# Performance work log

Hardware: AMD Instinct MI355X
Metric: run time of the kernel (lower is better)

Reference implementation:

```python
import jax, jax.numpy as jnp
import numpy as np

B, T, DIN, DOUT = 32, 3136, 192, 384
H, QS, WS = 6, 4, 16            # heads, q_stride, window_size (post-pool)
HD = DOUT // H                   # head_dim = 64
INNER = QS * WS                  # tokens per mask unit before pooling = 64
NW = T // INNER                  # num_windows = 49
MLP_HID = 4 * DOUT
EPS = 1e-5


def layer_norm(x, w, b):
    mu = x.mean(-1, keepdims=True)
    var = ((x - mu) ** 2).mean(-1, keepdims=True)
    return (x - mu) * jax.lax.rsqrt(var + EPS) * w + b


def setup_inputs() -> dict:
    key = jax.random.key(0)
    ks = jax.random.split(key, 16)
    rn = lambda k, shp, fan: jax.random.normal(k, shp, jnp.float32) * (fan ** -0.5)
    return {
        "embeddings": jax.random.normal(ks[0], (B, T, DIN), jnp.float32),
        "norm1_w": jnp.ones((DIN,), jnp.float32),
        "norm1_b": jnp.zeros((DIN,), jnp.float32),
        "w_qkv": rn(ks[1], (3 * DOUT, DIN), DIN),
        "b_qkv": jnp.zeros((3 * DOUT,), jnp.float32),
        "w_attn_proj": rn(ks[2], (DOUT, DOUT), DOUT),
        "b_attn_proj": jnp.zeros((DOUT,), jnp.float32),
        "w_res_proj": rn(ks[3], (DOUT, DIN), DIN),
        "b_res_proj": jnp.zeros((DOUT,), jnp.float32),
        "norm2_w": jnp.ones((DOUT,), jnp.float32),
        "norm2_b": jnp.zeros((DOUT,), jnp.float32),
        "w_fc1": rn(ks[4], (MLP_HID, DOUT), DOUT),
        "b_fc1": jnp.zeros((MLP_HID,), jnp.float32),
        "w_fc2": rn(ks[5], (DOUT, MLP_HID), MLP_HID),
        "b_fc2": jnp.zeros((DOUT,), jnp.float32),
    }


def _block(embeddings, norm1_w, norm1_b, w_qkv, b_qkv, w_attn_proj, b_attn_proj,
           w_res_proj, b_res_proj, norm2_w, norm2_b, w_fc1, b_fc1, w_fc2, b_fc2):
    x = layer_norm(embeddings, norm1_w, norm1_b)                 # [B,T,DIN]

    # residual path: project then do_pool (max over q_stride groups)
    res = x @ w_res_proj.T + b_res_proj                          # [B,T,DOUT]
    res = res.reshape(B, QS, T // QS, DOUT).max(axis=1)          # [B,T/QS,DOUT]

    # mask-unit attention
    qkv = x @ w_qkv.T + b_qkv                                    # [B,T,3*DOUT]
    qkv = qkv.reshape(B, INNER, NW, 3, H, HD)
    qkv = jnp.transpose(qkv, (3, 0, 4, 2, 1, 5))                 # [3,B,H,NW,INNER,HD]
    q, k, v = qkv[0], qkv[1], qkv[2]
    q = q.reshape(B, H, NW, QS, WS, HD).max(axis=3)              # q-pool -> [B,H,NW,WS,HD]
    scale = HD ** -0.5
    attn = jax.nn.softmax(jnp.einsum("bhwqd,bhwkd->bhwqk", q * scale, k), axis=-1)
    out = jnp.einsum("bhwqk,bhwkd->bhwqd", attn, v)              # [B,H,NW,WS,HD]
    out = jnp.transpose(out, (0, 3, 2, 1, 4)).reshape(B, WS * NW, DOUT)
    out = out @ w_attn_proj.T + b_attn_proj

    emb = res + out
    h = layer_norm(emb, norm2_w, norm2_b)
    h = jax.nn.gelu(h @ w_fc1.T + b_fc1, approximate=False)
    emb = emb + (h @ w_fc2.T + b_fc2)
    return emb, attn


def reference(embeddings, norm1_w, norm1_b, w_qkv, b_qkv, w_attn_proj, b_attn_proj,
              w_res_proj, b_res_proj, norm2_w, norm2_b, w_fc1, b_fc1, w_fc2, b_fc2):
    return _block(embeddings, norm1_w, norm1_b, w_qkv, b_qkv, w_attn_proj, b_attn_proj,
                  w_res_proj, b_res_proj, norm2_w, norm2_b, w_fc1, b_fc1, w_fc2, b_fc2)
```

## Files before the change

kernel.cpp:

```cpp
#include <hip/hip_runtime.h>
#include <stdint.h>

typedef __bf16 bf16_t;
typedef __attribute__((ext_vector_type(8))) __bf16 bf16x8;
typedef __attribute__((ext_vector_type(4))) __bf16 bf16x4;
typedef __attribute__((ext_vector_type(4))) float f32x4;

#define NB_ 32
#define NT_ 3136
#define DIN_ 192
#define DOUT_ 384
#define NH_ 6
#define HD_ 64
#define NW_ 49
#define WSZ_ 16
#define TP_ 784
#define MLP_ 1536

__device__ __forceinline__ f32x4 mfma16(bf16x8 a, bf16x8 b, f32x4 c) {
  return __builtin_amdgcn_mfma_f32_16x16x32_bf16(a, b, c, 0, 0, 0);
}

__device__ __forceinline__ void gload_lds16(const bf16_t* g, bf16_t* l) {
  __builtin_amdgcn_global_load_lds(
      (const __attribute__((address_space(1))) void*)((const void*)g),
      (__attribute__((address_space(3))) void*)l, 16, 0, 0);
}

__device__ __forceinline__ float gelu_tanh(float v) {
  const float t2 = 1.5957691216f * (v + 0.044715f * v * v * v);
  return v * (1.f - 1.f / (1.f + __expf(t2)));
}

__global__ void cvt_kernel(const float* __restrict__ s0, const float* __restrict__ s1,
                           const float* __restrict__ s2, const float* __restrict__ s3,
                           const float* __restrict__ s4, bf16_t* __restrict__ d0,
                           bf16_t* __restrict__ d1, bf16_t* __restrict__ d2,
                           bf16_t* __restrict__ d3, bf16_t* __restrict__ d4) {
  const int b = blockIdx.x;
  const float* s; bf16_t* d; long off;
  if (b < 108)      { s = s0; d = d0; off = (long)b * 2048; }
  else if (b < 144) { s = s1; d = d1; off = (long)(b - 108) * 2048; }
  else if (b < 216) { s = s2; d = d2; off = (long)(b - 144) * 2048; }
  else if (b < 504) { s = s3; d = d3; off = (long)(b - 216) * 2048; }
  else              { s = s4; d = d4; off = (long)(b - 504) * 2048; }
  off += (long)threadIdx.x * 8;
  const float4 a = *(const float4*)(s + off);
  const float4 c = *(const float4*)(s + off + 4);
  bf16x8 o;
  o[0] = (bf16_t)a.x; o[1] = (bf16_t)a.y; o[2] = (bf16_t)a.z; o[3] = (bf16_t)a.w;
  o[4] = (bf16_t)c.x; o[5] = (bf16_t)c.y; o[6] = (bf16_t)c.z; o[7] = (bf16_t)c.w;
  *(bf16x8*)(d + off) = o;
}

template <int D>
__global__ void ln_f32_kernel(const float* __restrict__ in, const float* __restrict__ w,
                              const float* __restrict__ bvec, bf16_t* __restrict__ out) {
  const int row = blockIdx.x * 4 + (threadIdx.x >> 6);
  const int lane = threadIdx.x & 63;
  constexpr int PER = D / 64;
  const float* x = in + (long)row * D;
  float v[PER];
  float s = 0.f;
#pragma unroll
  for (int i = 0; i < PER; i++) { v[i] = x[lane * PER + i]; s += v[i]; }
#pragma unroll
  for (int off = 1; off < 64; off <<= 1) s += __shfl_xor(s, off);
  const float mu = s * (1.f / D);
  float s2 = 0.f;
#pragma unroll
  for (int i = 0; i < PER; i++) { const float d = v[i] - mu; s2 += d * d; }
#pragma unroll
  for (int off = 1; off < 64; off <<= 1) s2 += __shfl_xor(s2, off);
  const float rstd = rsqrtf(s2 * (1.f / D) + 1e-5f);
  bf16_t* o = out + (long)row * D;
#pragma unroll
  for (int i = 0; i < PER; i++) {
    const int c = lane * PER + i;
    o[c] = (bf16_t)((v[i] - mu) * rstd * w[c] + bvec[c]);
  }
}

template <int D>
__global__ void ln_bf16_kernel(const bf16_t* __restrict__ in, const float* __restrict__ w,
                               const float* __restrict__ bvec, bf16_t* __restrict__ out) {
  const int row = blockIdx.x * 4 + (threadIdx.x >> 6);
  const int lane = threadIdx.x & 63;
  constexpr int PER = D / 64;
  const bf16_t* x = in + (long)row * D;
  float v[PER];
  float s = 0.f;
#pragma unroll
  for (int i = 0; i < PER; i++) { v[i] = (float)x[lane * PER + i]; s += v[i]; }
#pragma unroll
  for (int off = 1; off < 64; off <<= 1) s += __shfl_xor(s, off);
  const float mu = s * (1.f / D);
  float s2 = 0.f;
#pragma unroll
  for (int i = 0; i < PER; i++) { const float d = v[i] - mu; s2 += d * d; }
#pragma unroll
  for (int off = 1; off < 64; off <<= 1) s2 += __shfl_xor(s2, off);
  const float rstd = rsqrtf(s2 * (1.f / D) + 1e-5f);
  bf16_t* o = out + (long)row * D;
#pragma unroll
  for (int i = 0; i < PER; i++) {
    const int c = lane * PER + i;
    o[c] = (bf16_t)((v[i] - mu) * rstd * w[c] + bvec[c]);
  }
}

template <int ACT, int POOL>
__global__ __launch_bounds__(512, 4) void gemm8(
    const bf16_t* __restrict__ A, const bf16_t* __restrict__ W,
    const float* __restrict__ bias, bf16_t* __restrict__ C,
    int M, int N, int K) {
  __shared__ __align__(16) char AsB[256 * 128];
  __shared__ __align__(16) char WsB[128 * 128];

  const int nwg = gridDim.x;
  const int q = nwg >> 3, rm = nwg & 7;
  const int xcd = blockIdx.x & 7, idx = blockIdx.x >> 3;
  const int wg = (xcd < rm ? xcd * (q + 1) : rm * (q + 1) + (xcd - rm) * q) + idx;

  const int nbn = N >> 7;
  const int bmi = wg / nbn;
  const int bni = wg - bmi * nbn;
  const int m0 = bmi << 8, n0 = bni << 7;
  const int tid = threadIdx.x;
  const int lane = tid & 63;
  const int wid = tid >> 6;
  const int wr = (wid >> 1) * 64, wc = (wid & 1) * 64;
  const int l15 = lane & 15;
  const int lkb = (lane >> 4) << 4;
  const int srow = tid >> 3;
  const int scolsw = ((tid & 7) << 3) ^ ((srow & 7) << 3);
  const int swzr = (l15 & 7) << 4;

  f32x4 acc[4][4];
  const f32x4 zero = {0.f, 0.f, 0.f, 0.f};
#pragma unroll
  for (int i = 0; i < 4; i++)
#pragma unroll
    for (int j = 0; j < 4; j++) acc[i][j] = zero;

  long arow[4];
#pragma unroll
  for (int p = 0; p < 4; p++) {
    const int m = m0 + p * 64 + srow;
    if constexpr (POOL) {
      const int b = m / NT_;
      const int mm = m - b * NT_;
      arow[p] = (long)b * NT_ + (mm & 3) * TP_ + (mm >> 2);
    } else {
      arow[p] = m;
    }
  }
  long wrow[2];
#pragma unroll
  for (int p = 0; p < 2; p++) wrow[p] = (long)(n0 + p * 64 + srow);

  for (int k0 = 0; k0 < K; k0 += 64) {
    __syncthreads();
#pragma unroll
    for (int p = 0; p < 4; p++)
      gload_lds16(A + arow[p] * K + k0 + scolsw, (bf16_t*)(AsB + p * 8192 + tid * 16));
#pragma unroll
    for (int p = 0; p < 2; p++)
      gload_lds16(W + wrow[p] * K + k0 + scolsw, (bf16_t*)(WsB + p * 8192 + tid * 16));
    __syncthreads();
#pragma unroll
    for (int kk = 0; kk < 2; kk++) {
      bf16x8 af[4], wf[4];
#pragma unroll
      for (int i = 0; i < 4; i++)
        af[i] = *(const bf16x8*)(AsB + (wr + i * 16 + l15) * 128 + ((kk * 64 + lkb) ^ swzr));
#pragma unroll
      for (int j = 0; j < 4; j++)
        wf[j] = *(const bf16x8*)(WsB + (wc + j * 16 + l15) * 128 + ((kk * 64 + lkb) ^ swzr));
#pragma unroll
      for (int i = 0; i < 4; i++)
#pragma unroll
        for (int j = 0; j < 4; j++) {
          if constexpr (POOL) acc[i][j] = mfma16(af[i], wf[j], acc[i][j]);
          else                acc[i][j] = mfma16(wf[j], af[i], acc[i][j]);
        }
    }
  }

  const int rg = (lane >> 4) * 4;
  if constexpr (POOL) {
#pragma unroll
    for (int j = 0; j < 4; j++) {
      const int gn = n0 + wc + j * 16 + l15;
      const float bv = bias[gn];
#pragma unroll
      for (int i = 0; i < 4; i++) {
        const float v = fmaxf(fmaxf(acc[i][j][0], acc[i][j][1]),
                              fmaxf(acc[i][j][2], acc[i][j][3])) + bv;
        const long pm = (long)((m0 + wr + i * 16 + rg) >> 2);
        C[pm * N + gn] = (bf16_t)v;
      }
    }
  } else {
    __syncthreads();
    char* scr = AsB + wid * 4096;
#pragma unroll
    for (int i = 0; i < 4; i++) {
#pragma unroll
      for (int j = 0; j < 4; j++)
        *(f32x4*)(scr + l15 * 256 + ((((j * 16 + rg) << 2)) ^ ((l15 & 7) << 4))) = acc[i][j];
#pragma unroll
      for (int k = 0; k < 4; k++) {
        const int rl = k * 4 + (lane >> 4);
        const int cb = (lane & 15) << 4;
        const f32x4 v = *(const f32x4*)(scr + rl * 256 + (cb ^ ((rl & 7) << 4)));
        const long gm = m0 + wr + i * 16 + rl;
        const int gn = n0 + wc + ((lane & 15) << 2);
        const float4 bv = *(const float4*)(bias + gn);
        float vv[4] = {v[0] + bv.x, v[1] + bv.y, v[2] + bv.z, v[3] + bv.w};
        if constexpr (ACT == 1) {
#pragma unroll
          for (int r = 0; r < 4; r++) vv[r] = gelu_tanh(vv[r]);
        }
        bf16x4 o;
#pragma unroll
        for (int r = 0; r < 4; r++) o[r] = (bf16_t)vv[r];
        *(bf16x4*)(C + gm * N + gn) = o;
      }
    }
  }
}

template <int HASRES, int OF32, int RF32>
__global__ __launch_bounds__(256) void gemm_t(
    const bf16_t* __restrict__ A, const bf16_t* __restrict__ W,
    const float* __restrict__ bias, const void* __restrict__ resv,
    void* __restrict__ Cv, int M, int N, int K) {
  constexpr int BM = 64;
  constexpr int PA = BM / 32;
  constexpr int ABYTES = BM * 128;
  constexpr int BUFSZ = ABYTES + 128 * 128;
  __shared__ __align__(16) char LDSB[2 * BUFSZ];

  const int nwg = gridDim.x;
  const int q = nwg >> 3, rm = nwg & 7;
  const int xcd = blockIdx.x & 7, idx = blockIdx.x >> 3;
  const int wg = (xcd < rm ? xcd * (q + 1) : rm * (q + 1) + (xcd - rm) * q) + idx;

  const int nbn = N >> 7;
  const int bmi = wg / nbn;
  const int bni = wg - bmi * nbn;
  const int m0 = bmi * BM, n0 = bni << 7;
  const int tid = threadIdx.x;
  const int lane = tid & 63;
  const int wid = tid >> 6;
  const int wr = (wid >> 1) * 32, wc = (wid & 1) * 64;
  const int l15 = lane & 15;
  const int lkb = (lane >> 4) << 4;
  const int srow = tid >> 3;
  const int scolsw = ((tid & 7) << 3) ^ ((srow & 7) << 3);
  const int swzr = (l15 & 7) << 4;

  f32x4 acc[PA][4];
  const f32x4 zero = {0.f, 0.f, 0.f, 0.f};
#pragma unroll
  for (int i = 0; i < PA; i++)
#pragma unroll
    for (int j = 0; j < 4; j++) acc[i][j] = zero;

  long arow[PA];
#pragma unroll
  for (int p = 0; p < PA; p++) arow[p] = m0 + srow + p * 32;
  long wrow[4];
#pragma unroll
  for (int p = 0; p < 4; p++) wrow[p] = (long)(n0 + srow + p * 32);

  auto stage = [&](int buf, int k0) {
    char* base = LDSB + buf * BUFSZ;
#pragma unroll
    for (int p = 0; p < PA; p++)
      gload_lds16(A + arow[p] * K + k0 + scolsw, (bf16_t*)(base + p * 4096 + tid * 16));
#pragma unroll
    for (int p = 0; p < 4; p++)
      gload_lds16(W + wrow[p] * K + k0 + scolsw,
                  (bf16_t*)(base + ABYTES + p * 4096 + tid * 16));
  };

  const int nt = K >> 6;
  stage(0, 0);
  int cur = 0;
  for (int t = 0; t < nt; t++) {
    __syncthreads();
    if (t + 1 < nt) stage(cur ^ 1, (t + 1) << 6);
    const char* base = LDSB + cur * BUFSZ;
#pragma unroll
    for (int kk = 0; kk < 2; kk++) {
      bf16x8 af[PA], wf[4];
#pragma unroll
      for (int i = 0; i < PA; i++)
        af[i] = *(const bf16x8*)(base + (wr + i * 16 + l15) * 128 + ((kk * 64 + lkb) ^ swzr));
#pragma unroll
      for (int j = 0; j < 4; j++)
        wf[j] = *(const bf16x8*)(base + ABYTES + (wc + j * 16 + l15) * 128 +
                                 ((kk * 64 + lkb) ^ swzr));
#pragma unroll
      for (int i = 0; i < PA; i++)
#pragma unroll
        for (int j = 0; j < 4; j++) acc[i][j] = mfma16(wf[j], af[i], acc[i][j]);
    }
    cur ^= 1;
  }

  __syncthreads();
  char* scr = LDSB + wid * 8192;
  const int rg = (lane >> 4) * 4;
#pragma unroll
  for (int i = 0; i < PA; i++) {
    const int ml = i * 16 + l15;
#pragma unroll
    for (int j = 0; j < 4; j++)
      *(f32x4*)(scr + ml * 256 + ((((j * 16 + rg) << 2)) ^ ((ml & 7) << 4))) = acc[i][j];
  }
#pragma unroll
  for (int k = 0; k < 8; k++) {
    const int rl = k * 4 + (lane >> 4);
    const int cb = (lane & 15) << 4;
    const f32x4 v = *(const f32x4*)(scr + rl * 256 + (cb ^ ((rl & 7) << 4)));
    const long gm = m0 + wr + rl;
    const int gn = n0 + wc + ((lane & 15) << 2);
    const float4 bv = *(const float4*)(bias + gn);
    float vv[4] = {v[0] + bv.x, v[1] + bv.y, v[2] + bv.z, v[3] + bv.w};
    if constexpr (HASRES) {
      if constexpr (RF32) {
        const float4 rv = *(const float4*)((const float*)resv + gm * N + gn);
        vv[0] += rv.x; vv[1] += rv.y; vv[2] += rv.z; vv[3] += rv.w;
      } else {
        const bf16x4 rv = *(const bf16x4*)((const bf16_t*)resv + gm * N + gn);
#pragma unroll
        for (int r = 0; r < 4; r++) vv[r] += (float)rv[r];
      }
    }
    if constexpr (OF32) {
      float4 o = {vv[0], vv[1], vv[2], vv[3]};
      *(float4*)((float*)Cv + gm * N + gn) = o;
    } else {
      bf16x4 o;
#pragma unroll
      for (int r = 0; r < 4; r++) o[r] = (bf16_t)vv[r];
      *(bf16x4*)((bf16_t*)Cv + gm * N + gn) = o;
    }
  }
}

__global__ __launch_bounds__(256) void attn_kernel(const bf16_t* __restrict__ qkv,
                                                   float* __restrict__ attn_out,
                                                   bf16_t* __restrict__ obuf) {
  __shared__ __align__(16) bf16_t Vs[4][64 * 64];
  __shared__ __align__(16) bf16_t Ps[4][16 * 64];
  const int wid = threadIdx.x >> 6;
  const int lane = threadIdx.x & 63;
  const int flat = blockIdx.x * 4 + wid;
  const int w = flat % NW_;
  const int h = (flat / NW_) % NH_;
  const int b = flat / (NW_ * NH_);
  const int l15 = lane & 15, lk8 = (lane >> 4) * 8;
  const bf16_t* qb = qkv + (long)b * NT_ * (3 * DOUT_);
  bf16_t* Vw = Vs[wid];
  bf16_t* Pw = Ps[wid];

#pragma unroll
  for (int p = 0; p < 8; p++) {
    const int inner = p * 8 + (lane >> 3);
    const int col = (lane & 7) * 8;
    const bf16x8 t =
        *(const bf16x8*)(qb + (long)(inner * NW_ + w) * (3 * DOUT_) + 2 * DOUT_ + h * HD_ + col);
    *(bf16x8*)&Vw[p * 512 + lane * 8] = t;
  }

  bf16x8 aq[2];
#pragma unroll
  for (int kc = 0; kc < 2; kc++) {
    const int d = kc * 32 + lk8;
    float qv[8];
#pragma unroll
    for (int e = 0; e < 8; e++) qv[e] = -1e30f;
#pragma unroll
    for (int qs = 0; qs < 4; qs++) {
      const bf16x8 t =
          *(const bf16x8*)(qb + (long)((qs * 16 + l15) * NW_ + w) * (3 * DOUT_) + h * HD_ + d);
#pragma unroll
      for (int e = 0; e < 8; e++) qv[e] = fmaxf(qv[e], (float)t[e]);
    }
    bf16x8 a;
#pragma unroll
    for (int e = 0; e < 8; e++) a[e] = (bf16_t)(qv[e] * 0.125f);
    aq[kc] = a;
  }

  f32x4 s4[4];
  const f32x4 zero = {0.f, 0.f, 0.f, 0.f};
#pragma unroll
  for (int nc = 0; nc < 4; nc++) s4[nc] = zero;
#pragma unroll
  for (int nc = 0; nc < 4; nc++) {
#pragma unroll
    for (int kc = 0; kc < 2; kc++) {
      const int tok = nc * 16 + l15;
      const int d = kc * 32 + lk8;
      const bf16x8 bk =
          *(const bf16x8*)(qb + (long)(tok * NW_ + w) * (3 * DOUT_) + DOUT_ + h * HD_ + d);
      s4[nc] = mfma16(aq[kc], bk, s4[nc]);
    }
  }

#pragma unroll
  for (int r = 0; r < 4; r++) {
    float mx = fmaxf(fmaxf(s4[0][r], s4[1][r]), fmaxf(s4[2][r], s4[3][r]));
#pragma unroll
    for (int off = 1; off < 16; off <<= 1) mx = fmaxf(mx, __shfl_xor(mx, off));
    float sm = 0.f;
#pragma unroll
    for (int nc = 0; nc < 4; nc++) {
      const float p = __expf(s4[nc][r] - mx);
      s4[nc][r] = p;
      sm += p;
    }
#pragma unroll
    for (int off = 1; off < 16; off <<= 1) sm += __shfl_xor(sm, off);
    const float inv = 1.f / sm;
#pragma unroll
    for (int nc = 0; nc < 4; nc++) s4[nc][r] *= inv;
  }

  const int rg = (lane >> 4) * 4;
  float* aout = attn_out + (long)flat * (WSZ_ * 64);
#pragma unroll
  for (int nc = 0; nc < 4; nc++) {
#pragma unroll
    for (int r = 0; r < 4; r++) {
      const int row = rg + r, col = nc * 16 + l15;
      aout[row * 64 + col] = s4[nc][r];
      Pw[row * 64 + col] = (bf16_t)s4[nc][r];
    }
  }

  bf16x8 ap[2];
#pragma unroll
  for (int kc = 0; kc < 2; kc++) ap[kc] = *(const bf16x8*)&Pw[l15 * 64 + kc * 32 + lk8];

  f32x4 o4[4];
#pragma unroll
  for (int nc = 0; nc < 4; nc++) o4[nc] = zero;
#pragma unroll
  for (int nc = 0; nc < 4; nc++) {
#pragma unroll
    for (int kc = 0; kc < 2; kc++) {
      bf16x8 bv;
#pragma unroll
      for (int e = 0; e < 8; e++) bv[e] = Vw[(kc * 32 + lk8 + e) * 64 + nc * 16 + l15];
      o4[nc] = mfma16(ap[kc], bv, o4[nc]);
    }
  }

  bf16_t* ob = obuf + (long)b * TP_ * DOUT_;
#pragma unroll
  for (int nc = 0; nc < 4; nc++) {
#pragma unroll
    for (int r = 0; r < 4; r++) {
      const int wsr = rg + r;
      const int tprime = wsr * NW_ + w;
      const int chan = h * HD_ + nc * 16 + l15;
      ob[(long)tprime * DOUT_ + chan] = (bf16_t)o4[nc][r];
    }
  }
}

extern "C" void kernel_launch(void* const* d_in, const int* in_sizes, int n_in,
                              void* d_out, int out_size, void* d_ws, size_t ws_size,
                              hipStream_t stream) {
  const float* emb   = (const float*)d_in[0];
  const float* n1w   = (const float*)d_in[1];
  const float* n1b   = (const float*)d_in[2];
  const float* wqkv  = (const float*)d_in[3];
  const float* bqkv  = (const float*)d_in[4];
  const float* wproj = (const float*)d_in[5];
  const float* bproj = (const float*)d_in[6];
  const float* wres  = (const float*)d_in[7];
  const float* bres  = (const float*)d_in[8];
  const float* n2w   = (const float*)d_in[9];
  const float* n2b   = (const float*)d_in[10];
  const float* wfc1  = (const float*)d_in[11];
  const float* bfc1  = (const float*)d_in[12];
  const float* wfc2  = (const float*)d_in[13];
  const float* bfc2  = (const float*)d_in[14];
  float* out = (float*)d_out;

  const int BT = NB_ * NT_;
  const int BTP = NB_ * TP_;
  const int BSL = 8;
  const int MSL = BSL * NT_;

  char* wsb = (char*)d_ws;
  bf16_t* qkvb = (bf16_t*)(wsb);
  bf16_t* h1   = (bf16_t*)(wsb);
  bf16_t* obuf = (bf16_t*)(wsb + 57802752L);
  bf16_t* resp = (bf16_t*)(wsb + 77070336L);
  bf16_t* h0   = resp;
  bf16_t* emb1 = (bf16_t*)(wsb + 96337920L);
  bf16_t* wbqkv = (bf16_t*)(wsb + 115605504L);
  bf16_t* wbres = wbqkv + 221184L;
  bf16_t* wbproj = wbres + 73728L;
  bf16_t* wbfc1 = wbproj + 147456L;
  bf16_t* wbfc2 = wbfc1 + 589824L;
  float*  prob = out + 9633792L;
  bf16_t* x    = (bf16_t*)(out + 9633792L);

  cvt_kernel<<<792, 256, 0, stream>>>(wqkv, wres, wproj, wfc1, wfc2,
                                      wbqkv, wbres, wbproj, wbfc1, wbfc2);
  ln_f32_kernel<DIN_><<<BT / 4, 256, 0, stream>>>(emb, n1w, n1b, x);
  gemm8<0, 1><<<(BT / 256) * (DOUT_ / 128), 512, 0, stream>>>(
      x, wbres, bres, resp, BT, DOUT_, DIN_);
  for (int s = 0; s < 4; s++) {
    gemm8<0, 0><<<(MSL / 256) * (3 * DOUT_ / 128), 512, 0, stream>>>(
        x + (long)s * MSL * DIN_, wbqkv, bqkv, qkvb, MSL, 3 * DOUT_, DIN_);
    attn_kernel<<<BSL * NH_ * NW_ / 4, 256, 0, stream>>>(
        qkvb, prob + (long)s * 2408448L, obuf + (long)s * 2408448L);
  }
  gemm_t<1, 0, 0><<<(BTP / 64) * (DOUT_ / 128), 256, 0, stream>>>(
      obuf, wbproj, bproj, resp, emb1, BTP, DOUT_, DOUT_);
  ln_bf16_kernel<DOUT_><<<BTP / 4, 256, 0, stream>>>(emb1, n2w, n2b, h0);
  gemm8<1, 0><<<(BTP / 256) * (MLP_ / 128), 512, 0, stream>>>(
      h0, wbfc1, bfc1, h1, BTP, MLP_, DOUT_);
  gemm_t<1, 1, 0><<<(BTP / 64) * (DOUT_ / 128), 256, 0, stream>>>(
      h1, wbfc2, bfc2, emb1, out, BTP, DOUT_, MLP_);
}
```

Baseline: 332.3 us.

## Fuse QKV projection into mask-unit attention kernel, drop QKV buffer

```diff
diff --git a/kernel.cpp b/kernel.cpp
--- a/kernel.cpp
+++ b/kernel.cpp
@@ -352,64 +352,114 @@
   }
 }
 
-__global__ __launch_bounds__(256) void attn_kernel(const bf16_t* __restrict__ qkv,
-                                                   float* __restrict__ attn_out,
-                                                   bf16_t* __restrict__ obuf) {
-  __shared__ __align__(16) bf16_t Vs[4][64 * 64];
-  __shared__ __align__(16) bf16_t Ps[4][16 * 64];
-  const int wid = threadIdx.x >> 6;
-  const int lane = threadIdx.x & 63;
-  const int flat = blockIdx.x * 4 + wid;
-  const int w = flat % NW_;
-  const int h = (flat / NW_) % NH_;
-  const int b = flat / (NW_ * NH_);
-  const int l15 = lane & 15, lk8 = (lane >> 4) * 8;
-  const bf16_t* qb = qkv + (long)b * NT_ * (3 * DOUT_);
-  bf16_t* Vw = Vs[wid];
-  bf16_t* Pw = Ps[wid];
-
-#pragma unroll
-  for (int p = 0; p < 8; p++) {
-    const int inner = p * 8 + (lane >> 3);
-    const int col = (lane & 7) * 8;
-    const bf16x8 t =
-        *(const bf16x8*)(qb + (long)(inner * NW_ + w) * (3 * DOUT_) + 2 * DOUT_ + h * HD_ + col);
-    *(bf16x8*)&Vw[p * 512 + lane * 8] = t;
-  }
-
+__global__ __launch_bounds__(384) void qkv_attn_kernel(
+    const bf16_t* __restrict__ x, const bf16_t* __restrict__ Wqkv,
+    const float* __restrict__ bq, float* __restrict__ prob,
+    bf16_t* __restrict__ obuf) {
+  __shared__ __align__(16) char As[64 * 384];
+  __shared__ __align__(16) char Qs[6][2048];
+  __shared__ __align__(16) char Kb[6][4096];
+  const int b = blockIdx.x / NW_;
+  const int w = blockIdx.x - b * NW_;
+  const int tid = threadIdx.x;
+  const int lane = tid & 63;
+  const int h = tid >> 6;
+  const int l15 = lane & 15;
+  const int lk8 = (lane >> 4) * 8;
+  const int lkb = (lane >> 4) << 4;
+  const int rg = (lane >> 4) * 4;
+  const f32x4 zero = {0.f, 0.f, 0.f, 0.f};
+
+#pragma unroll
+  for (int i = 0; i < 4; i++) {
+    const int row = i * 16 + tid / 24;
+    const int cb = ((tid % 24) * 16) ^ ((row & 7) << 4);
+    gload_lds16(x + ((long)b * NT_ + (long)row * NW_ + w) * DIN_ + cb / 2,
+                (bf16_t*)(As + i * 6144 + tid * 16));
+  }
+  __syncthreads();
+
+  char* Qw = Qs[h];
+  char* Bw = Kb[h];
+  auto gemm_part = [&](int which, f32x4 (&acc)[4][4]) {
+#pragma unroll
+    for (int i = 0; i < 4; i++)
+#pragma unroll
+      for (int j = 0; j < 4; j++) acc[i][j] = zero;
+#pragma unroll
+    for (int j = 0; j < 4; j++) {
+      const bf16_t* wrow = Wqkv + (long)(which * DOUT_ + h * HD_ + j * 16 + l15) * DIN_;
+      bf16x8 wf[6];
+#pragma unroll
+      for (int ks = 0; ks < 6; ks++)
+        wf[ks] = *(const bf16x8*)(wrow + ks * 32 + lk8);
+#pragma unroll
+      for (int ks = 0; ks < 6; ks++) {
+#pragma unroll
+        for (int i = 0; i < 4; i++) {
+          const int mr = i * 16 + l15;
+          const bf16x8 af = *(const bf16x8*)(As + mr * 384 +
+                                             ((ks * 64 + lkb) ^ ((mr & 7) << 4)));
+          acc[i][j] = mfma16(af, wf[ks], acc[i][j]);
+        }
+      }
+    }
+  };
+
+  f32x4 acc[4][4];
+  gemm_part(0, acc);
+#pragma unroll
+  for (int j = 0; j < 4; j++) {
+    const float bb = bq[h * HD_ + j * 16 + l15];
+#pragma unroll
+    for (int r = 0; r < 4; r++) {
+      const float v = (fmaxf(fmaxf(acc[0][j][r], acc[1][j][r]),
+                             fmaxf(acc[2][j][r], acc[3][j][r])) + bb) * 0.125f;
+      const int row = rg + r;
+      *(bf16_t*)(Qw + row * 128 + (((j * 16 + l15) * 2) ^ ((row & 7) << 4))) = (bf16_t)v;
+    }
+  }
   bf16x8 aq[2];
 #pragma unroll
-  for (int kc = 0; kc < 2; kc++) {
-    const int d = kc * 32 + lk8;
-    float qv[8];
-#pragma unroll
-    for (int e = 0; e < 8; e++) qv[e] = -1e30f;
-#pragma unroll
-    for (int qs = 0; qs < 4; qs++) {
-      const bf16x8 t =
-          *(const bf16x8*)(qb + (long)((qs * 16 + l15) * NW_ + w) * (3 * DOUT_) + h * HD_ + d);
-#pragma unroll
-      for (int e = 0; e < 8; e++) qv[e] = fmaxf(qv[e], (float)t[e]);
-    }
-    bf16x8 a;
-#pragma unroll
-    for (int e = 0; e < 8; e++) a[e] = (bf16_t)(qv[e] * 0.125f);
-    aq[kc] = a;
-  }
-
+  for (int kc = 0; kc < 2; kc++)
+    aq[kc] = *(const bf16x8*)(Qw + l15 * 128 + ((kc * 64 + lkb) ^ ((l15 & 7) << 4)));
+
+  gemm_part(1, acc);
+#pragma unroll
+  for (int j = 0; j < 4; j++) {
+    const float bb = bq[DOUT_ + h * HD_ + j * 16 + l15];
+#pragma unroll
+    for (int i = 0; i < 4; i++)
+#pragma unroll
+      for (int r = 0; r < 4; r++) acc[i][j][r] += bb;
+  }
   f32x4 s4[4];
-  const f32x4 zero = {0.f, 0.f, 0.f, 0.f};
 #pragma unroll
   for (int nc = 0; nc < 4; nc++) s4[nc] = zero;
 #pragma unroll
-  for (int nc = 0; nc < 4; nc++) {
-#pragma unroll
-    for (int kc = 0; kc < 2; kc++) {
-      const int tok = nc * 16 + l15;
-      const int d = kc * 32 + lk8;
-      const bf16x8 bk =
-          *(const bf16x8*)(qb + (long)(tok * NW_ + w) * (3 * DOUT_) + DOUT_ + h * HD_ + d);
-      s4[nc] = mfma16(aq[kc], bk, s4[nc]);
+  for (int t = 0; t < 2; t++) {
+#pragma unroll
+    for (int i2 = 0; i2 < 2; i2++) {
+      const int i = t * 2 + i2;
+#pragma unroll
+      for (int j = 0; j < 4; j++)
+#pragma unroll
+        for (int r = 0; r < 4; r++) {
+          const int tokh = i2 * 16 + rg + r;
+          *(bf16_t*)(Bw + tokh * 128 + (((j * 16 + l15) * 2) ^ ((tokh & 7) << 4))) =
+              (bf16_t)acc[i][j][r];
+        }
+    }
+#pragma unroll
+    for (int nch = 0; nch < 2; nch++) {
+      const int nc = t * 2 + nch;
+      const int tokh = nch * 16 + l15;
+#pragma unroll
+      for (int kc = 0; kc < 2; kc++) {
+        const bf16x8 bk = *(const bf16x8*)(Bw + tokh * 128 +
+                                           ((kc * 64 + lkb) ^ ((tokh & 7) << 4)));
+        s4[nc] = mfma16(aq[kc], bk, s4[nc]);
+      }
     }
   }
 
@@ -432,33 +482,57 @@
     for (int nc = 0; nc < 4; nc++) s4[nc][r] *= inv;
   }
 
-  const int rg = (lane >> 4) * 4;
-  float* aout = attn_out + (long)flat * (WSZ_ * 64);
+  float* aout = prob + (long)((b * NH_ + h) * NW_ + w) * (WSZ_ * 64);
 #pragma unroll
   for (int nc = 0; nc < 4; nc++) {
 #pragma unroll
     for (int r = 0; r < 4; r++) {
       const int row = rg + r, col = nc * 16 + l15;
       aout[row * 64 + col] = s4[nc][r];
-      Pw[row * 64 + col] = (bf16_t)s4[nc][r];
-    }
-  }
-
+      *(bf16_t*)(Qw + row * 128 + ((col * 2) ^ ((row & 7) << 4))) = (bf16_t)s4[nc][r];
+    }
+  }
   bf16x8 ap[2];
 #pragma unroll
-  for (int kc = 0; kc < 2; kc++) ap[kc] = *(const bf16x8*)&Pw[l15 * 64 + kc * 32 + lk8];
-
+  for (int kc = 0; kc < 2; kc++)
+    ap[kc] = *(const bf16x8*)(Qw + l15 * 128 + ((kc * 64 + lkb) ^ ((l15 & 7) << 4)));
+
+  gemm_part(2, acc);
+#pragma unroll
+  for (int j = 0; j < 4; j++) {
+    const float bb = bq[2 * DOUT_ + h * HD_ + j * 16 + l15];
+#pragma unroll
+    for (int i = 0; i < 4; i++)
+#pragma unroll
+      for (int r = 0; r < 4; r++) acc[i][j][r] += bb;
+  }
   f32x4 o4[4];
 #pragma unroll
   for (int nc = 0; nc < 4; nc++) o4[nc] = zero;
 #pragma unroll
-  for (int nc = 0; nc < 4; nc++) {
-#pragma unroll
-    for (int kc = 0; kc < 2; kc++) {
+  for (int t = 0; t < 2; t++) {
+#pragma unroll
+    for (int i2 = 0; i2 < 2; i2++) {
+      const int i = t * 2 + i2;
+#pragma unroll
+      for (int j = 0; j < 4; j++)
+#pragma unroll
+        for (int r = 0; r < 4; r++) {
+          const int tokh = i2 * 16 + rg + r;
+          *(bf16_t*)(Bw + tokh * 128 + (((j * 16 + l15) * 2) ^ ((tokh & 7) << 4))) =
+              (bf16_t)acc[i][j][r];
+        }
+    }
+#pragma unroll
+    for (int nc = 0; nc < 4; nc++) {
       bf16x8 bv;
 #pragma unroll
-      for (int e = 0; e < 8; e++) bv[e] = Vw[(kc * 32 + lk8 + e) * 64 + nc * 16 + l15];
-      o4[nc] = mfma16(ap[kc], bv, o4[nc]);
+      for (int e = 0; e < 8; e++) {
+        const int tokh = lk8 + e;
+        bv[e] = *(const bf16_t*)(Bw + tokh * 128 +
+                                 (((nc * 16 + l15) * 2) ^ ((tokh & 7) << 4)));
+      }
+      o4[nc] = mfma16(ap[t], bv, o4[nc]);
     }
   }
 
@@ -497,11 +571,9 @@
 
   const int BT = NB_ * NT_;
   const int BTP = NB_ * TP_;
-  const int BSL = 8;
-  const int MSL = BSL * NT_;
 
   char* wsb = (char*)d_ws;
-  bf16_t* qkvb = (bf16_t*)(wsb);
+  bf16_t* x    = (bf16_t*)(wsb);
   bf16_t* h1   = (bf16_t*)(wsb);
   bf16_t* obuf = (bf16_t*)(wsb + 57802752L);
   bf16_t* resp = (bf16_t*)(wsb + 77070336L);
@@ -513,19 +585,13 @@
   bf16_t* wbfc1 = wbproj + 147456L;
   bf16_t* wbfc2 = wbfc1 + 589824L;
   float*  prob = out + 9633792L;
-  bf16_t* x    = (bf16_t*)(out + 9633792L);
 
   cvt_kernel<<<792, 256, 0, stream>>>(wqkv, wres, wproj, wfc1, wfc2,
                                       wbqkv, wbres, wbproj, wbfc1, wbfc2);
   ln_f32_kernel<DIN_><<<BT / 4, 256, 0, stream>>>(emb, n1w, n1b, x);
   gemm8<0, 1><<<(BT / 256) * (DOUT_ / 128), 512, 0, stream>>>(
       x, wbres, bres, resp, BT, DOUT_, DIN_);
-  for (int s = 0; s < 4; s++) {
-    gemm8<0, 0><<<(MSL / 256) * (3 * DOUT_ / 128), 512, 0, stream>>>(
-        x + (long)s * MSL * DIN_, wbqkv, bqkv, qkvb, MSL, 3 * DOUT_, DIN_);
-    attn_kernel<<<BSL * NH_ * NW_ / 4, 256, 0, stream>>>(
-        qkvb, prob + (long)s * 2408448L, obuf + (long)s * 2408448L);
-  }
+  qkv_attn_kernel<<<NB_ * NW_, 384, 0, stream>>>(x, wbqkv, bqkv, prob, obuf);
   gemm_t<1, 0, 0><<<(BTP / 64) * (DOUT_ / 128), 256, 0, stream>>>(
       obuf, wbproj, bproj, resp, emb1, BTP, DOUT_, DOUT_);
   ln_bf16_kernel<DOUT_><<<BTP / 4, 256, 0, stream>>>(emb1, n2w, n2b, h0);
```

Measured after the change: 312.8 us. -5.9%, faster.
